# Optimization experiments

Hardware: AMD Instinct MI355X
Metric: run time of the kernel (lower is better)

The kernel has to match this reference:

```python
import jax, jax.numpy as jnp
import numpy as np

N_SAMPLES = 200
HASHMAP = 1 << 19  # 2^19 hashmap size cap per level
P1, P2, P3 = 1, 2654435761, 805459861  # spatial hash primes


def _levels(base, n):
    res = [base * (2 ** l) for l in range(n)]
    sizes = [min(r ** 3, HASHMAP) for r in res]
    off = np.concatenate([[0], np.cumsum(sizes)])
    return res, off


def grid_encode(x, table, base, n):
    # x: [M,3] in [-1,1]; table: [sum(level_sizes), level_dim]
    x01 = jnp.clip((x + 1.0) * 0.5, 0.0, 1.0)
    res_l, off = _levels(base, n)
    outs = []
    for l, res in enumerate(res_l):
        dense = (res ** 3) <= HASHMAP
        pos = x01 * (res - 1)
        g = jnp.clip(jnp.floor(pos), 0, res - 2).astype(jnp.uint32)
        f = pos - g.astype(x01.dtype)
        feat = 0.0
        for cx in (0, 1):
            for cy in (0, 1):
                for cz in (0, 1):
                    c0, c1, c2 = g[:, 0] + cx, g[:, 1] + cy, g[:, 2] + cz
                    if dense:
                        idx = (c0 * res + c1) * res + c2
                    else:
                        idx = (c0 * jnp.uint32(P1)) ^ (c1 * jnp.uint32(P2)) ^ (c2 * jnp.uint32(P3))
                        idx = idx & jnp.uint32(HASHMAP - 1)
                    wx = f[:, 0] if cx else 1.0 - f[:, 0]
                    wy = f[:, 1] if cy else 1.0 - f[:, 1]
                    wz = f[:, 2] if cz else 1.0 - f[:, 2]
                    feat = feat + (wx * wy * wz)[:, None] * table[int(off[l]) + idx.astype(jnp.int32)]
        outs.append(feat)
    return jnp.concatenate(outs, axis=-1)


def sample_points_along_ray(x):
    # x: [N,4] = (theta1, phi1, theta2, phi2)
    def sph2cart(theta, phi):
        st = jnp.sin(theta)
        return jnp.stack([st * jnp.cos(phi), st * jnp.sin(phi), jnp.cos(theta)], axis=-1)
    t = jnp.linspace(0.0, 1.0, N_SAMPLES).reshape(1, N_SAMPLES, 1)
    p1 = sph2cart(x[:, 0], x[:, 1])
    p2 = sph2cart(x[:, 2], x[:, 3])
    diff = p2 - p1
    points = p1[:, None, :] + diff[:, None, :] * t  # [N,200,3]
    norm = jnp.clip(jnp.linalg.norm(diff, axis=-1, keepdims=True), 1e-6, 1e6)
    return points, diff / norm


def setup_inputs() -> dict:
    key = jax.random.key(0)
    ks = jax.random.split(key, 16)
    B = 32768
    x = jax.random.uniform(ks[0], (B, 4)) * jnp.array([np.pi, 2 * np.pi, np.pi, 2 * np.pi], jnp.float32)
    label_sz = sum(min((8 * 2 ** l) ** 3, HASHMAP) for l in range(6))   # 1348096
    rgb_sz = sum(min((4 * 2 ** l) ** 3, HASHMAP) for l in range(5))     # 299584
    def lin(k, fi, fo):
        return jax.random.normal(k, (fi, fo)) / np.sqrt(fi)
    return {
        'x': x,
        'label_table': jax.random.uniform(ks[1], (label_sz, 1), minval=-1e-4, maxval=1e-4),
        'label_w': lin(ks[2], 6, 1), 'label_b': jnp.zeros((1,)),
        'rgb_table': jax.random.uniform(ks[3], (rgb_sz, 4), minval=-1e-4, maxval=1e-4),
        'w1': lin(ks[4], 23, 64), 'b1': jnp.zeros((64,)),
        'w2': lin(ks[5], 64, 64), 'b2': jnp.zeros((64,)),
        'w3': lin(ks[6], 64, 64), 'b3': jnp.zeros((64,)),
        'w4': lin(ks[7], 64, 3), 'b4': jnp.zeros((3,)),
    }


def reference(x, label_table, label_w, label_b, rgb_table, w1, b1, w2, b2, w3, b3, w4, b4):
    N = x.shape[0]
    points, dirs = sample_points_along_ray(x)
    points = jax.lax.stop_gradient(points)   # torch.no_grad in original
    dirs = jax.lax.stop_gradient(dirs)
    pflat = points.reshape(-1, 3)            # [N*200, 3]
    enc_label = grid_encode(pflat, label_table, 8, 6).reshape(N, N_SAMPLES, 6)
    output = jax.nn.sigmoid(enc_label @ label_w + label_b)        # [N,200,1]
    output_hits = jnp.max(output, axis=1)                          # [N,1]
    enc_rgb = grid_encode(pflat, rgb_table, 4, 5).reshape(N, N_SAMPLES, 20)
    all_labels = jax.lax.stop_gradient((output > 0.5).astype(output.dtype))
    idx_first = jnp.clip(jnp.argmax(all_labels, axis=1).reshape(-1), 2, N_SAMPLES - 3)  # [N]
    sel = jnp.take_along_axis(enc_rgb, idx_first[:, None, None], axis=1)[:, 0, :]       # [N,20]
    feat = jnp.concatenate([dirs, sel], axis=-1)                   # [N,23]
    h = jax.nn.relu(feat @ w1 + b1)
    h = jax.nn.relu(h @ w2 + b2)
    h = jax.nn.relu(h @ w3 + b3)
    output_rgb = h @ w4 + b4                                       # [N,3]
    return output_hits, output, idx_first, output_rgb
```

## Files before the change

kernel.cpp:

```cpp
#include <hip/hip_runtime.h>
#include <math.h>

#define NSAMP 200

__device__ __forceinline__ float sin_f32cr(float x) { return (float)sin((double)x); }
__device__ __forceinline__ float cos_f32cr(float x) { return (float)cos((double)x); }

template <bool DENSE>
__device__ __forceinline__ float enc_level_f(float x0, float y0, float z0,
                                             int res, const float* __restrict__ tbl) {
    const float rf = (float)(res - 1);
    const float px = __fmul_rn(x0, rf);
    const float py = __fmul_rn(y0, rf);
    const float pz = __fmul_rn(z0, rf);
    const float gmax = (float)(res - 2);
    const float gxf = fminf(fmaxf(floorf(px), 0.0f), gmax);
    const float gyf = fminf(fmaxf(floorf(py), 0.0f), gmax);
    const float gzf = fminf(fmaxf(floorf(pz), 0.0f), gmax);
    const float fx = __fsub_rn(px, gxf);
    const float fy = __fsub_rn(py, gyf);
    const float fz = __fsub_rn(pz, gzf);
    const unsigned gx = (unsigned)gxf, gy = (unsigned)gyf, gz = (unsigned)gzf;
    const float wx[2] = {__fsub_rn(1.0f, fx), fx};
    const float wy[2] = {__fsub_rn(1.0f, fy), fy};
    const float wz[2] = {__fsub_rn(1.0f, fz), fz};
    float feat = 0.0f;
#pragma unroll
    for (int c = 0; c < 8; ++c) {
        const int cx = (c >> 2) & 1, cy = (c >> 1) & 1, cz = c & 1;
        const unsigned c0 = gx + cx, c1 = gy + cy, c2 = gz + cz;
        unsigned idx;
        if (DENSE) {
            idx = (c0 * (unsigned)res + c1) * (unsigned)res + c2;
        } else {
            idx = (c0 * 1u ^ c1 * 2654435761u ^ c2 * 805459861u) & 524287u;
        }
        const float w = __fmul_rn(__fmul_rn(wx[cx], wy[cy]), wz[cz]);
        feat = __fadd_rn(feat, __fmul_rn(w, tbl[idx]));
    }
    return feat;
}

__device__ __forceinline__ float clamp01f(float v) {
    return fminf(fmaxf(v, 0.0f), 1.0f);
}

__global__ __launch_bounds__(256)
void fused_nerf(const float* __restrict__ x,
                const float* __restrict__ lbl_tbl,
                const float* __restrict__ lbl_w,
                const float* __restrict__ lbl_b,
                const float* __restrict__ rgb_tbl,
                const float* __restrict__ w1, const float* __restrict__ b1,
                const float* __restrict__ w2, const float* __restrict__ b2,
                const float* __restrict__ w3, const float* __restrict__ b3,
                const float* __restrict__ w4, const float* __restrict__ b4,
                float* __restrict__ out_hits,
                float* __restrict__ out_sig,
                float* __restrict__ out_idx,
                float* __restrict__ out_rgb,
                int N)
{
    const int wid = blockIdx.x * 4 + ((int)threadIdx.x >> 6);
    const int lane = (int)threadIdx.x & 63;
    if (wid >= N) return;

    const float th1 = x[wid * 4 + 0], ph1 = x[wid * 4 + 1];
    const float th2 = x[wid * 4 + 2], ph2 = x[wid * 4 + 3];
    const float st1 = sin_f32cr(th1), ct1 = cos_f32cr(th1);
    const float sp1 = sin_f32cr(ph1), cp1 = cos_f32cr(ph1);
    const float st2 = sin_f32cr(th2), ct2 = cos_f32cr(th2);
    const float sp2 = sin_f32cr(ph2), cp2 = cos_f32cr(ph2);
    const float p1x = __fmul_rn(st1, cp1), p1y = __fmul_rn(st1, sp1), p1z = ct1;
    const float p2x = __fmul_rn(st2, cp2), p2y = __fmul_rn(st2, sp2), p2z = ct2;
    const float dx = __fsub_rn(p2x, p1x), dy = __fsub_rn(p2y, p1y), dz = __fsub_rn(p2z, p1z);
    const float n2 = __fadd_rn(__fadd_rn(__fmul_rn(dx, dx), __fmul_rn(dy, dy)), __fmul_rn(dz, dz));
    float nrm = fminf(fmaxf(__fsqrt_rn(n2), 1e-6f), 1e6f);
    const float dirx = __fdiv_rn(dx, nrm), diry = __fdiv_rn(dy, nrm), dirz = __fdiv_rn(dz, nrm);

    const float lw0 = lbl_w[0], lw1 = lbl_w[1], lw2 = lbl_w[2];
    const float lw3 = lbl_w[3], lw4_ = lbl_w[4], lw5 = lbl_w[5];
    const float lb = lbl_b[0];

    const float stepf = 1.0f / 199.0f;

    float maxsig = -1e30f;
    int minidx = 1 << 30;

    for (int s = lane; s < NSAMP; s += 64) {
        const float t = __fmul_rn((float)s, stepf);
        const float px = __fadd_rn(p1x, __fmul_rn(dx, t));
        const float py = __fadd_rn(p1y, __fmul_rn(dy, t));
        const float pz = __fadd_rn(p1z, __fmul_rn(dz, t));
        const float x0 = clamp01f(__fmul_rn(__fadd_rn(px, 1.0f), 0.5f));
        const float y0 = clamp01f(__fmul_rn(__fadd_rn(py, 1.0f), 0.5f));
        const float z0 = clamp01f(__fmul_rn(__fadd_rn(pz, 1.0f), 0.5f));

        const float f0 = enc_level_f<true >(x0, y0, z0,   8, lbl_tbl + 0     );
        const float f1 = enc_level_f<true >(x0, y0, z0,  16, lbl_tbl + 512   );
        const float f2 = enc_level_f<true >(x0, y0, z0,  32, lbl_tbl + 4608  );
        const float f3 = enc_level_f<true >(x0, y0, z0,  64, lbl_tbl + 37376 );
        const float f4 = enc_level_f<false>(x0, y0, z0, 128, lbl_tbl + 299520);
        const float f5 = enc_level_f<false>(x0, y0, z0, 256, lbl_tbl + 823808);

        float acc = __fmul_rn(f0, lw0);
        acc = __fadd_rn(acc, __fmul_rn(f1, lw1));
        acc = __fadd_rn(acc, __fmul_rn(f2, lw2));
        acc = __fadd_rn(acc, __fmul_rn(f3, lw3));
        acc = __fadd_rn(acc, __fmul_rn(f4, lw4_));
        acc = __fadd_rn(acc, __fmul_rn(f5, lw5));
        const float z = __fadd_rn(acc, lb);

        const float e = (float)exp(-(double)z);
        const float sig = __fdiv_rn(1.0f, __fadd_rn(1.0f, e));

        out_sig[wid * NSAMP + s] = sig;
        maxsig = fmaxf(maxsig, sig);
        if (sig > 0.5f && s < minidx) minidx = s;
    }

#pragma unroll
    for (int d = 1; d < 64; d <<= 1) {
        maxsig = fmaxf(maxsig, __shfl_xor(maxsig, d));
        minidx = min(minidx, __shfl_xor(minidx, d));
    }
    int idxf = (minidx >= NSAMP) ? 0 : minidx;
    idxf = min(max(idxf, 2), 197);
    if (lane == 0) {
        out_hits[wid] = maxsig;
        out_idx[wid] = (float)idxf;
    }

    const float tt = __fmul_rn((float)idxf, stepf);
    const float qx = __fadd_rn(p1x, __fmul_rn(dx, tt));
    const float qy = __fadd_rn(p1y, __fmul_rn(dy, tt));
    const float qz = __fadd_rn(p1z, __fmul_rn(dz, tt));
    const float rx0 = clamp01f(__fmul_rn(__fadd_rn(qx, 1.0f), 0.5f));
    const float ry0 = clamp01f(__fmul_rn(__fadd_rn(qy, 1.0f), 0.5f));
    const float rz0 = clamp01f(__fmul_rn(__fadd_rn(qz, 1.0f), 0.5f));

    float ax = 0.0f, ay = 0.0f, az = 0.0f, aw = 0.0f;
    if (lane < 40) {
        const int L = lane >> 3, c = lane & 7;
        const int res = 4 << L;
        const unsigned off = (64u * ((1u << (3 * L)) - 1u)) / 7u;
        const float rf = (float)(res - 1);
        const float pxp = __fmul_rn(rx0, rf);
        const float pyp = __fmul_rn(ry0, rf);
        const float pzp = __fmul_rn(rz0, rf);
        const float gmax = (float)(res - 2);
        const float gxf = fminf(fmaxf(floorf(pxp), 0.0f), gmax);
        const float gyf = fminf(fmaxf(floorf(pyp), 0.0f), gmax);
        const float gzf = fminf(fmaxf(floorf(pzp), 0.0f), gmax);
        const float fx = __fsub_rn(pxp, gxf);
        const float fy = __fsub_rn(pyp, gyf);
        const float fz = __fsub_rn(pzp, gzf);
        const unsigned gx = (unsigned)gxf, gy = (unsigned)gyf, gz = (unsigned)gzf;
        const int cx = (c >> 2) & 1, cy = (c >> 1) & 1, cz = c & 1;
        const unsigned idx = ((gx + cx) * (unsigned)res + (gy + cy)) * (unsigned)res + (gz + cz);
        const float4 v = *reinterpret_cast<const float4*>(rgb_tbl + 4u * (off + idx));
        const float w = __fmul_rn(__fmul_rn(cx ? fx : __fsub_rn(1.0f, fx),
                                            cy ? fy : __fsub_rn(1.0f, fy)),
                                  cz ? fz : __fsub_rn(1.0f, fz));
        ax = w * v.x; ay = w * v.y; az = w * v.z; aw = w * v.w;
    }
#pragma unroll
    for (int d = 1; d <= 4; d <<= 1) {
        ax += __shfl_xor(ax, d);
        ay += __shfl_xor(ay, d);
        az += __shfl_xor(az, d);
        aw += __shfl_xor(aw, d);
    }
    float sel[20];
#pragma unroll
    for (int L = 0; L < 5; ++L) {
        sel[4 * L + 0] = __shfl(ax, 8 * L);
        sel[4 * L + 1] = __shfl(ay, 8 * L);
        sel[4 * L + 2] = __shfl(az, 8 * L);
        sel[4 * L + 3] = __shfl(aw, 8 * L);
    }

    float h = b1[lane];
    h += dirx * w1[0 * 64 + lane];
    h += diry * w1[1 * 64 + lane];
    h += dirz * w1[2 * 64 + lane];
#pragma unroll
    for (int k = 0; k < 20; ++k) h += sel[k] * w1[(3 + k) * 64 + lane];
    h = fmaxf(h, 0.0f);

    float h2 = b2[lane];
#pragma unroll 8
    for (int k = 0; k < 64; ++k) h2 += __shfl(h, k) * w2[k * 64 + lane];
    h2 = fmaxf(h2, 0.0f);

    float h3 = b3[lane];
#pragma unroll 8
    for (int k = 0; k < 64; ++k) h3 += __shfl(h2, k) * w3[k * 64 + lane];
    h3 = fmaxf(h3, 0.0f);

    float o0 = h3 * w4[lane * 3 + 0];
    float o1 = h3 * w4[lane * 3 + 1];
    float o2 = h3 * w4[lane * 3 + 2];
#pragma unroll
    for (int d = 1; d < 64; d <<= 1) {
        o0 += __shfl_xor(o0, d);
        o1 += __shfl_xor(o1, d);
        o2 += __shfl_xor(o2, d);
    }
    if (lane == 0) {
        out_rgb[wid * 3 + 0] = o0 + b4[0];
        out_rgb[wid * 3 + 1] = o1 + b4[1];
        out_rgb[wid * 3 + 2] = o2 + b4[2];
    }
}

extern "C" void kernel_launch(void* const* d_in, const int* in_sizes, int n_in,
                              void* d_out, int out_size, void* d_ws, size_t ws_size,
                              hipStream_t stream) {
    const float* x        = (const float*)d_in[0];
    const float* lbl_tbl  = (const float*)d_in[1];
    const float* lbl_w    = (const float*)d_in[2];
    const float* lbl_b    = (const float*)d_in[3];
    const float* rgb_tbl  = (const float*)d_in[4];
    const float* w1       = (const float*)d_in[5];
    const float* b1       = (const float*)d_in[6];
    const float* w2       = (const float*)d_in[7];
    const float* b2       = (const float*)d_in[8];
    const float* w3       = (const float*)d_in[9];
    const float* b3       = (const float*)d_in[10];
    const float* w4       = (const float*)d_in[11];
    const float* b4       = (const float*)d_in[12];

    const int N = in_sizes[0] / 4;

    float* out = (float*)d_out;
    float* out_hits = out;
    float* out_sig  = out + N;
    float* out_idx  = out + N + N * NSAMP;
    float* out_rgb  = out + N + N * NSAMP + N;

    dim3 grid((N + 3) / 4), block(256);
    hipLaunchKernelGGL(fused_nerf, grid, block, 0, stream,
                       x, lbl_tbl, lbl_w, lbl_b, rgb_tbl,
                       w1, b1, w2, b2, w3, b3, w4, b4,
                       out_hits, out_sig, out_idx, out_rgb, N);
}
```

Measured before the change: 358.3 us.

## Split fused NeRF kernel into ray-setup, per-sample label, and finish passes

Splits the single fused kernel into three launches. The first computes per-ray endpoints and directions into a workspace. The second runs one thread per sample, fixing the old lane imbalance where 200 samples over 64 lanes left most lanes idle on the fourth iteration, and it issues all 48 table gathers up front to expose memory-level parallelism. The third rereads sigma from global memory for the max/argmax reduction and runs the RGB MLP. The cost is two extra kernel launches, an extra read of the sigma buffer, and higher register pressure from the 48-entry arrays.

New measurement: 347.3 us. 3.1% less time.

```diff
diff --git a/kernel.cpp b/kernel.cpp
--- a/kernel.cpp
+++ b/kernel.cpp
@@ -2,13 +2,19 @@
 #include <math.h>
 
 #define NSAMP 200
+#define RAY_STRIDE 12
 
 __device__ __forceinline__ float sin_f32cr(float x) { return (float)sin((double)x); }
 __device__ __forceinline__ float cos_f32cr(float x) { return (float)cos((double)x); }
 
+__device__ __forceinline__ float clamp01f(float v) {
+    return fminf(fmaxf(v, 0.0f), 1.0f);
+}
+
 template <bool DENSE>
-__device__ __forceinline__ float enc_level_f(float x0, float y0, float z0,
-                                             int res, const float* __restrict__ tbl) {
+__device__ __forceinline__ void enc_idx(float x0, float y0, float z0, int res,
+                                        unsigned base, unsigned* __restrict__ idx,
+                                        float* __restrict__ w) {
     const float rf = (float)(res - 1);
     const float px = __fmul_rn(x0, rf);
     const float py = __fmul_rn(y0, rf);
@@ -24,49 +30,28 @@
     const float wx[2] = {__fsub_rn(1.0f, fx), fx};
     const float wy[2] = {__fsub_rn(1.0f, fy), fy};
     const float wz[2] = {__fsub_rn(1.0f, fz), fz};
-    float feat = 0.0f;
 #pragma unroll
     for (int c = 0; c < 8; ++c) {
         const int cx = (c >> 2) & 1, cy = (c >> 1) & 1, cz = c & 1;
         const unsigned c0 = gx + cx, c1 = gy + cy, c2 = gz + cz;
-        unsigned idx;
+        unsigned id;
         if (DENSE) {
-            idx = (c0 * (unsigned)res + c1) * (unsigned)res + c2;
+            id = (c0 * (unsigned)res + c1) * (unsigned)res + c2;
         } else {
-            idx = (c0 * 1u ^ c1 * 2654435761u ^ c2 * 805459861u) & 524287u;
+            id = (c0 * 1u ^ c1 * 2654435761u ^ c2 * 805459861u) & 524287u;
         }
-        const float w = __fmul_rn(__fmul_rn(wx[cx], wy[cy]), wz[cz]);
-        feat = __fadd_rn(feat, __fmul_rn(w, tbl[idx]));
-    }
-    return feat;
-}
-
-__device__ __forceinline__ float clamp01f(float v) {
-    return fminf(fmaxf(v, 0.0f), 1.0f);
+        idx[c] = base + id;
+        w[c] = __fmul_rn(__fmul_rn(wx[cx], wy[cy]), wz[cz]);
+    }
 }
 
 __global__ __launch_bounds__(256)
-void fused_nerf(const float* __restrict__ x,
-                const float* __restrict__ lbl_tbl,
-                const float* __restrict__ lbl_w,
-                const float* __restrict__ lbl_b,
-                const float* __restrict__ rgb_tbl,
-                const float* __restrict__ w1, const float* __restrict__ b1,
-                const float* __restrict__ w2, const float* __restrict__ b2,
-                const float* __restrict__ w3, const float* __restrict__ b3,
-                const float* __restrict__ w4, const float* __restrict__ b4,
-                float* __restrict__ out_hits,
-                float* __restrict__ out_sig,
-                float* __restrict__ out_idx,
-                float* __restrict__ out_rgb,
-                int N)
+void ray_setup(const float* __restrict__ x, float* __restrict__ ws, int N)
 {
-    const int wid = blockIdx.x * 4 + ((int)threadIdx.x >> 6);
-    const int lane = (int)threadIdx.x & 63;
-    if (wid >= N) return;
-
-    const float th1 = x[wid * 4 + 0], ph1 = x[wid * 4 + 1];
-    const float th2 = x[wid * 4 + 2], ph2 = x[wid * 4 + 3];
+    const int r = blockIdx.x * 256 + (int)threadIdx.x;
+    if (r >= N) return;
+    const float th1 = x[r * 4 + 0], ph1 = x[r * 4 + 1];
+    const float th2 = x[r * 4 + 2], ph2 = x[r * 4 + 3];
     const float st1 = sin_f32cr(th1), ct1 = cos_f32cr(th1);
     const float sp1 = sin_f32cr(ph1), cp1 = cos_f32cr(ph1);
     const float st2 = sin_f32cr(th2), ct2 = cos_f32cr(th2);
@@ -75,50 +60,104 @@
     const float p2x = __fmul_rn(st2, cp2), p2y = __fmul_rn(st2, sp2), p2z = ct2;
     const float dx = __fsub_rn(p2x, p1x), dy = __fsub_rn(p2y, p1y), dz = __fsub_rn(p2z, p1z);
     const float n2 = __fadd_rn(__fadd_rn(__fmul_rn(dx, dx), __fmul_rn(dy, dy)), __fmul_rn(dz, dz));
-    float nrm = fminf(fmaxf(__fsqrt_rn(n2), 1e-6f), 1e6f);
-    const float dirx = __fdiv_rn(dx, nrm), diry = __fdiv_rn(dy, nrm), dirz = __fdiv_rn(dz, nrm);
-
-    const float lw0 = lbl_w[0], lw1 = lbl_w[1], lw2 = lbl_w[2];
-    const float lw3 = lbl_w[3], lw4_ = lbl_w[4], lw5 = lbl_w[5];
-    const float lb = lbl_b[0];
+    const float nrm = fminf(fmaxf(__fsqrt_rn(n2), 1e-6f), 1e6f);
+    float* o = ws + (size_t)r * RAY_STRIDE;
+    o[0] = p1x; o[1] = p1y; o[2] = p1z;
+    o[3] = dx;  o[4] = dy;  o[5] = dz;
+    o[6] = __fdiv_rn(dx, nrm);
+    o[7] = __fdiv_rn(dy, nrm);
+    o[8] = __fdiv_rn(dz, nrm);
+}
+
+__global__ __launch_bounds__(256)
+void label_pass(const float* __restrict__ ws,
+                const float* __restrict__ lbl_tbl,
+                const float* __restrict__ lbl_w,
+                const float* __restrict__ lbl_b,
+                float* __restrict__ out_sig,
+                unsigned TOT)
+{
+    const unsigned gs = blockIdx.x * 256u + threadIdx.x;
+    if (gs >= TOT) return;
+    const unsigned r = gs / 200u;
+    const unsigned s = gs - r * 200u;
+
+    const float* rp = ws + (size_t)r * RAY_STRIDE;
+    const float p1x = rp[0], p1y = rp[1], p1z = rp[2];
+    const float dx = rp[3], dy = rp[4], dz = rp[5];
 
     const float stepf = 1.0f / 199.0f;
+    const float t = __fmul_rn((float)s, stepf);
+    const float px = __fadd_rn(p1x, __fmul_rn(dx, t));
+    const float py = __fadd_rn(p1y, __fmul_rn(dy, t));
+    const float pz = __fadd_rn(p1z, __fmul_rn(dz, t));
+    const float x0 = clamp01f(__fmul_rn(__fadd_rn(px, 1.0f), 0.5f));
+    const float y0 = clamp01f(__fmul_rn(__fadd_rn(py, 1.0f), 0.5f));
+    const float z0 = clamp01f(__fmul_rn(__fadd_rn(pz, 1.0f), 0.5f));
+
+    unsigned idx48[48];
+    float w48[48];
+    enc_idx<true >(x0, y0, z0,   8,      0u, idx48 +  0, w48 +  0);
+    enc_idx<true >(x0, y0, z0,  16,    512u, idx48 +  8, w48 +  8);
+    enc_idx<true >(x0, y0, z0,  32,   4608u, idx48 + 16, w48 + 16);
+    enc_idx<true >(x0, y0, z0,  64,  37376u, idx48 + 24, w48 + 24);
+    enc_idx<false>(x0, y0, z0, 128, 299520u, idx48 + 32, w48 + 32);
+    enc_idx<false>(x0, y0, z0, 256, 823808u, idx48 + 40, w48 + 40);
+
+    float v48[48];
+#pragma unroll
+    for (int i = 0; i < 48; ++i) v48[i] = lbl_tbl[idx48[i]];
+
+    float f[6];
+#pragma unroll
+    for (int l = 0; l < 6; ++l) {
+        float fe = 0.0f;
+#pragma unroll
+        for (int c = 0; c < 8; ++c)
+            fe = __fadd_rn(fe, __fmul_rn(w48[l * 8 + c], v48[l * 8 + c]));
+        f[l] = fe;
+    }
+    float acc = __fmul_rn(f[0], lbl_w[0]);
+    acc = __fadd_rn(acc, __fmul_rn(f[1], lbl_w[1]));
+    acc = __fadd_rn(acc, __fmul_rn(f[2], lbl_w[2]));
+    acc = __fadd_rn(acc, __fmul_rn(f[3], lbl_w[3]));
+    acc = __fadd_rn(acc, __fmul_rn(f[4], lbl_w[4]));
+    acc = __fadd_rn(acc, __fmul_rn(f[5], lbl_w[5]));
+    const float z = __fadd_rn(acc, lbl_b[0]);
+
+    const float e = (float)exp(-(double)z);
+    out_sig[gs] = __fdiv_rn(1.0f, __fadd_rn(1.0f, e));
+}
+
+__global__ __launch_bounds__(256)
+void finish_pass(const float* __restrict__ ws,
+                 const float* __restrict__ out_sig,
+                 const float* __restrict__ rgb_tbl,
+                 const float* __restrict__ w1, const float* __restrict__ b1,
+                 const float* __restrict__ w2, const float* __restrict__ b2,
+                 const float* __restrict__ w3, const float* __restrict__ b3,
+                 const float* __restrict__ w4, const float* __restrict__ b4,
+                 float* __restrict__ out_hits,
+                 float* __restrict__ out_idx,
+                 float* __restrict__ out_rgb,
+                 int N)
+{
+    const int wid = blockIdx.x * 4 + ((int)threadIdx.x >> 6);
+    const int lane = (int)threadIdx.x & 63;
+    if (wid >= N) return;
+
+    const float* rp = ws + (size_t)wid * RAY_STRIDE;
+    const float p1x = rp[0], p1y = rp[1], p1z = rp[2];
+    const float dx = rp[3], dy = rp[4], dz = rp[5];
+    const float dirx = rp[6], diry = rp[7], dirz = rp[8];
 
     float maxsig = -1e30f;
     int minidx = 1 << 30;
-
     for (int s = lane; s < NSAMP; s += 64) {
-        const float t = __fmul_rn((float)s, stepf);
-        const float px = __fadd_rn(p1x, __fmul_rn(dx, t));
-        const float py = __fadd_rn(p1y, __fmul_rn(dy, t));
-        const float pz = __fadd_rn(p1z, __fmul_rn(dz, t));
-        const float x0 = clamp01f(__fmul_rn(__fadd_rn(px, 1.0f), 0.5f));
-        const float y0 = clamp01f(__fmul_rn(__fadd_rn(py, 1.0f), 0.5f));
-        const float z0 = clamp01f(__fmul_rn(__fadd_rn(pz, 1.0f), 0.5f));
-
-        const float f0 = enc_level_f<true >(x0, y0, z0,   8, lbl_tbl + 0     );
-        const float f1 = enc_level_f<true >(x0, y0, z0,  16, lbl_tbl + 512   );
-        const float f2 = enc_level_f<true >(x0, y0, z0,  32, lbl_tbl + 4608  );
-        const float f3 = enc_level_f<true >(x0, y0, z0,  64, lbl_tbl + 37376 );
-        const float f4 = enc_level_f<false>(x0, y0, z0, 128, lbl_tbl + 299520);
-        const float f5 = enc_level_f<false>(x0, y0, z0, 256, lbl_tbl + 823808);
-
-        float acc = __fmul_rn(f0, lw0);
-        acc = __fadd_rn(acc, __fmul_rn(f1, lw1));
-        acc = __fadd_rn(acc, __fmul_rn(f2, lw2));
-        acc = __fadd_rn(acc, __fmul_rn(f3, lw3));
-        acc = __fadd_rn(acc, __fmul_rn(f4, lw4_));
-        acc = __fadd_rn(acc, __fmul_rn(f5, lw5));
-        const float z = __fadd_rn(acc, lb);
-
-        const float e = (float)exp(-(double)z);
-        const float sig = __fdiv_rn(1.0f, __fadd_rn(1.0f, e));
-
-        out_sig[wid * NSAMP + s] = sig;
-        maxsig = fmaxf(maxsig, sig);
-        if (sig > 0.5f && s < minidx) minidx = s;
-    }
-
+        const float sg = out_sig[wid * NSAMP + s];
+        maxsig = fmaxf(maxsig, sg);
+        if (sg > 0.5f && s < minidx) minidx = s;
+    }
 #pragma unroll
     for (int d = 1; d < 64; d <<= 1) {
         maxsig = fmaxf(maxsig, __shfl_xor(maxsig, d));
@@ -131,6 +170,7 @@
         out_idx[wid] = (float)idxf;
     }
 
+    const float stepf = 1.0f / 199.0f;
     const float tt = __fmul_rn((float)idxf, stepf);
     const float qx = __fadd_rn(p1x, __fmul_rn(dx, tt));
     const float qy = __fadd_rn(p1y, __fmul_rn(dy, tt));
@@ -232,6 +272,7 @@
     const float* b4       = (const float*)d_in[12];
 
     const int N = in_sizes[0] / 4;
+    const unsigned TOT = (unsigned)N * NSAMP;
 
     float* out = (float*)d_out;
     float* out_hits = out;
@@ -239,9 +280,13 @@
     float* out_idx  = out + N + N * NSAMP;
     float* out_rgb  = out + N + N * NSAMP + N;
 
-    dim3 grid((N + 3) / 4), block(256);
-    hipLaunchKernelGGL(fused_nerf, grid, block, 0, stream,
-                       x, lbl_tbl, lbl_w, lbl_b, rgb_tbl,
+    float* ws = (float*)d_ws;
+
+    hipLaunchKernelGGL(ray_setup, dim3((N + 255) / 256), dim3(256), 0, stream, x, ws, N);
+    hipLaunchKernelGGL(label_pass, dim3((TOT + 255u) / 256u), dim3(256), 0, stream,
+                       ws, lbl_tbl, lbl_w, lbl_b, out_sig, TOT);
+    hipLaunchKernelGGL(finish_pass, dim3((N + 3) / 4), dim3(256), 0, stream,
+                       ws, out_sig, rgb_tbl,
                        w1, b1, w2, b2, w3, b3, w4, b4,
-                       out_hits, out_sig, out_idx, out_rgb, N);
-}
+                       out_hits, out_idx, out_rgb, N);
+}
```
